# Kernel optimization log

Measured on AMD Instinct MI355X. Metric: run time of the kernel, lower is better.

The kernel has to match this reference:

```python
import jax, jax.numpy as jnp
import numpy as np

N_NODES = 200000   # total graph nodes (var + constraint)
N_VAR   = 112000   # nodes with x[:,0]==1, placed first for static slicing
N_EDGES = 3200000  # avg degree 16
HID     = 64
BATCH   = 64       # fc output width == batch_size in the torch module
TW      = 8        # target_width; TW*(TW-1)=56; N_VAR = seq_len*56 with seq_len=2000


def setup_inputs() -> dict:
    key = jax.random.key(0)
    ks = jax.random.split(key, 8)
    x = jax.random.normal(ks[0], (N_NODES, 2), jnp.float32)
    # var_mask = (x[:,0] == 1): make the first N_VAR nodes variable nodes.
    x = x.at[:, 0].set(jnp.where(jnp.arange(N_NODES) < N_VAR, 1.0, 0.0))
    edge_index = jax.random.randint(ks[1], (2, N_EDGES), 0, N_NODES, jnp.int32)
    W1 = jax.random.normal(ks[2], (2, HID), jnp.float32) / np.sqrt(2.0)
    b1 = jnp.zeros((HID,), jnp.float32)
    W2 = jax.random.normal(ks[3], (HID, HID), jnp.float32) / np.sqrt(HID)
    b2 = jnp.zeros((HID,), jnp.float32)
    Wfc = jax.random.normal(ks[4], (HID, BATCH), jnp.float32) / np.sqrt(HID)
    bfc = jnp.zeros((BATCH,), jnp.float32)
    return {"x": x, "edge_index": edge_index, "W1": W1, "b1": b1,
            "W2": W2, "b2": b2, "Wfc": Wfc, "bfc": bfc}


def gcn_conv(x, src, dst, W, b):
    """PyG GCNConv: transform, then sym-normalized aggregation with self-loops."""
    h = x @ W                                   # [N, F_out]
    ones = jnp.ones(src.shape[0], x.dtype)
    deg = jax.ops.segment_sum(ones, dst, num_segments=N_NODES) + 1.0  # +1: self-loop
    dinv = jax.lax.rsqrt(deg)                   # deg >= 1, always safe
    norm = dinv[src] * dinv[dst]                # [E]
    agg = jax.ops.segment_sum(h[src] * norm[:, None], dst, num_segments=N_NODES)
    agg = agg + h * (dinv * dinv)[:, None]      # self-loop message, norm = dinv_i^2
    return agg + b


def reference(x, edge_index, W1, b1, W2, b2, Wfc, bfc):
    src, dst = edge_index[0], edge_index[1]
    h = jax.nn.relu(gcn_conv(x, src, dst, W1, b1))
    h = gcn_conv(h, src, dst, W2, b2)
    # var_mask == first N_VAR rows by construction (static slice for jit)
    out = jax.nn.relu(h[:N_VAR] @ Wfc + bfc)    # [N_VAR, BATCH]
    width = TW * (TW - 1)                       # 56
    seq_len = N_VAR // width                    # 2000
    return jnp.round(out.reshape(seq_len, BATCH, width))
```

## Files before the change

### kernel.cpp

```cpp
#include <hip/hip_runtime.h>
#include <math.h>

#define N_NODES 200000
#define N_VAR   112000
#define N_EDGES 3200000
#define NB_SCAN 782
#define CAP     64

#define NFINE    512
#define PSZ_F    391
#define FCAP     7168
#define BIN_CHUNK 4096
#define NB_BIN   782

typedef int v4i __attribute__((ext_vector_type(4)));

__device__ __forceinline__ float bcast_lane(float x, int lane) {
    return __int_as_float(__builtin_amdgcn_readlane(__float_as_int(x), lane));
}

__global__ void __launch_bounds__(512) k_bin(const int* __restrict__ src,
                                             const int* __restrict__ dst,
                                             int* __restrict__ bins,
                                             int* __restrict__ bcnt,
                                             const float* __restrict__ W2,
                                             const float* __restrict__ b2,
                                             const float* __restrict__ Wfc,
                                             const float* __restrict__ bfc,
                                             float* __restrict__ Wc,
                                             float* __restrict__ bc) {
    __shared__ int hist[NFINE];
    __shared__ int seg[NFINE];
    __shared__ int gb[NFINE];
    __shared__ int cur[NFINE];
    __shared__ int wsum[8];
    __shared__ int stg[BIN_CHUNK];
    __shared__ unsigned short stgb[BIN_CHUNK];
    int tid = threadIdx.x;
    int lane = tid & 63, wid = tid >> 6;
    hist[tid] = 0;
    __syncthreads();

    int base = blockIdx.x * BIN_CHUNK;
    int pk[2][4];
    int bk[2][4];
    bool val[2];
    #pragma unroll
    for (int i = 0; i < 2; ++i) {
        int e4 = base + (i * 512 + tid) * 4;
        val[i] = (e4 < N_EDGES);
        if (val[i]) {
            v4i d = __builtin_nontemporal_load((const v4i*)(dst + e4));
            v4i s = __builtin_nontemporal_load((const v4i*)(src + e4));
            int dd[4] = {d.x, d.y, d.z, d.w};
            int ss[4] = {s.x, s.y, s.z, s.w};
            #pragma unroll
            for (int q = 0; q < 4; ++q) {
                int bb2 = dd[q] / PSZ_F;
                int dl = dd[q] - bb2 * PSZ_F;
                pk[i][q] = (dl << 18) | ss[q];
                bk[i][q] = bb2;
                atomicAdd(&hist[bb2], 1);
            }
        }
    }
    __syncthreads();

    int h = hist[tid];
    int inc = h;
    #pragma unroll
    for (int d = 1; d < 64; d <<= 1) {
        int t = __shfl_up(inc, d);
        if (lane >= d) inc += t;
    }
    if (lane == 63) wsum[wid] = inc;
    __syncthreads();
    int pre = 0, tot = 0;
    #pragma unroll
    for (int k = 0; k < 8; ++k) {
        int s = wsum[k];
        pre += (k < wid) ? s : 0;
        tot += s;
    }
    int ex = pre + inc - h;
    seg[tid] = ex;
    cur[tid] = ex;
    gb[tid]  = atomicAdd(&bcnt[tid], h);
    __syncthreads();

    #pragma unroll
    for (int i = 0; i < 2; ++i) {
        if (val[i]) {
            #pragma unroll
            for (int q = 0; q < 4; ++q) {
                int p = atomicAdd(&cur[bk[i][q]], 1);
                stg[p]  = pk[i][q];
                stgb[p] = (unsigned short)bk[i][q];
            }
        }
    }
    __syncthreads();

    for (int i = tid; i < tot; i += 512) {
        int bb2 = stgb[i];
        int pos = gb[bb2] + (i - seg[bb2]);
        if (pos < FCAP)
            bins[(size_t)bb2 * FCAP + pos] = stg[i];
    }

    int b = blockIdx.x;
    if (b < 8) {
        int e = b * 512 + tid;
        int j = e >> 6, l2 = e & 63;
        double acc = 0.0;
        for (int m = 0; m < 64; ++m)
            acc += (double)W2[j * 64 + m] * (double)Wfc[m * 64 + l2];
        Wc[e] = (float)acc;
    } else if (b == 8 && tid < 64) {
        double acc = (double)bfc[tid];
        for (int m = 0; m < 64; ++m)
            acc += (double)b2[m] * (double)Wfc[m * 64 + tid];
        bc[tid] = (float)acc;
    }
}

__global__ void __launch_bounds__(512) k_sort(const int* __restrict__ bins,
                                              const int* __restrict__ bcnt,
                                              const float2* __restrict__ x2,
                                              int* __restrict__ cnt,
                                              float4* __restrict__ xdc,
                                              int* __restrict__ buf) {
    __shared__ int hist[NFINE];
    __shared__ int off[NFINE];
    __shared__ int cur[NFINE];
    __shared__ int wsum[8];
    __shared__ int sorted[FCAP];
    __shared__ unsigned short rowid[FCAP];
    int tid = threadIdx.x;
    int lane = tid & 63, wid = tid >> 6;
    int b = blockIdx.x;
    int n = bcnt[b];
    if (n > FCAP) n = FCAP;
    const int* __restrict__ bp = bins + (size_t)b * FCAP;

    hist[tid] = 0;
    __syncthreads();
    for (int i = tid; i < n; i += 512)
        atomicAdd(&hist[bp[i] >> 18], 1);
    __syncthreads();

    int h = hist[tid];

    int vg = b * PSZ_F + tid;
    if (tid < PSZ_F && vg < N_NODES) {
        cnt[vg] = h;
        float dvv = rsqrtf((float)h + 1.0f);
        float2 xv = x2[vg];
        xdc[vg] = make_float4(xv.x * dvv, xv.y * dvv, dvv, 0.0f);
    }

    int inc = h;
    #pragma unroll
    for (int d = 1; d < 64; d <<= 1) {
        int t = __shfl_up(inc, d);
        if (lane >= d) inc += t;
    }
    if (lane == 63) wsum[wid] = inc;
    __syncthreads();
    int pre = 0;
    #pragma unroll
    for (int k = 0; k < 8; ++k) {
        int s = wsum[k];
        pre += (k < wid) ? s : 0;
    }
    int ex = pre + inc - h;
    off[tid] = ex;
    cur[tid] = ex;
    __syncthreads();

    for (int i = tid; i < n; i += 512) {
        int pkv = bp[i];
        int dl = pkv >> 18;
        int p = atomicAdd(&cur[dl], 1);
        sorted[p] = pkv & 0x3FFFF;
        rowid[p]  = (unsigned short)dl;
    }
    __syncthreads();

    for (int i = tid; i < n; i += 512) {
        int dl = rowid[i];
        int slot = i - off[dl];
        if (slot < CAP)
            buf[(size_t)(b * PSZ_F + dl) * CAP + slot] = sorted[i];
    }
}

__global__ void __launch_bounds__(256) k_l1a(const int* __restrict__ cnt,
                                             const int* __restrict__ buf,
                                             const float4* __restrict__ xdc,
                                             float4* __restrict__ zn) {
    int v = blockIdx.x * 256 + threadIdx.x;
    if (v >= N_NODES) return;
    int c = cnt[v];
    int n = (c < CAP) ? c : CAP;
    const int* __restrict__ rowp = buf + v * CAP;
    float4 self = xdc[v];
    float dv = self.z;
    float ax = self.x, ay = self.y;
    float bx = 0.0f,   by = 0.0f;
    int j = 0;
    for (; j + 16 <= n; j += 16) {
        v4i r0 = __builtin_nontemporal_load((const v4i*)(rowp + j));
        v4i r1 = __builtin_nontemporal_load((const v4i*)(rowp + j + 4));
        v4i r2 = __builtin_nontemporal_load((const v4i*)(rowp + j + 8));
        v4i r3 = __builtin_nontemporal_load((const v4i*)(rowp + j + 12));
        float4 p0 = xdc[r0.x], p1 = xdc[r0.y], p2 = xdc[r0.z], p3 = xdc[r0.w];
        float4 p4 = xdc[r1.x], p5 = xdc[r1.y], p6 = xdc[r1.z], p7 = xdc[r1.w];
        float4 p8 = xdc[r2.x], p9 = xdc[r2.y], pa = xdc[r2.z], pb = xdc[r2.w];
        float4 pc = xdc[r3.x], pd = xdc[r3.y], pe = xdc[r3.z], pf = xdc[r3.w];
        ax += p0.x; ay += p0.y;  bx += p1.x; by += p1.y;
        ax += p2.x; ay += p2.y;  bx += p3.x; by += p3.y;
        ax += p4.x; ay += p4.y;  bx += p5.x; by += p5.y;
        ax += p6.x; ay += p6.y;  bx += p7.x; by += p7.y;
        ax += p8.x; ay += p8.y;  bx += p9.x; by += p9.y;
        ax += pa.x; ay += pa.y;  bx += pb.x; by += pb.y;
        ax += pc.x; ay += pc.y;  bx += pd.x; by += pd.y;
        ax += pe.x; ay += pe.y;  bx += pf.x; by += pf.y;
    }
    for (; j + 8 <= n; j += 8) {
        v4i r0 = __builtin_nontemporal_load((const v4i*)(rowp + j));
        v4i r1 = __builtin_nontemporal_load((const v4i*)(rowp + j + 4));
        float4 p0 = xdc[r0.x], p1 = xdc[r0.y], p2 = xdc[r0.z], p3 = xdc[r0.w];
        float4 p4 = xdc[r1.x], p5 = xdc[r1.y], p6 = xdc[r1.z], p7 = xdc[r1.w];
        ax += p0.x; ay += p0.y;  bx += p1.x; by += p1.y;
        ax += p2.x; ay += p2.y;  bx += p3.x; by += p3.y;
        ax += p4.x; ay += p4.y;  bx += p5.x; by += p5.y;
        ax += p6.x; ay += p6.y;  bx += p7.x; by += p7.y;
    }
    for (; j < n; ++j) {
        int s = rowp[j];
        float4 p = xdc[s];
        ax += p.x; ay += p.y;
    }
    zn[v] = make_float4((ax + bx) * dv, (ay + by) * dv, dv, 0.0f);
}

__global__ void __launch_bounds__(256, 4) k_l2(const int* __restrict__ cnt,
                                               const int* __restrict__ buf,
                                               const float4* __restrict__ zn,
                                               const float* __restrict__ W1,
                                               const float* __restrict__ b1,
                                               const float* __restrict__ Wc,
                                               const float* __restrict__ bc,
                                               float* __restrict__ out) {
    int w = threadIdx.x >> 6, l = threadIdx.x & 63;
    float wc[64];
    #pragma unroll
    for (int jv = 0; jv < 64; ++jv)
        wc[jv] = Wc[jv * 64 + l];
    float w1a = W1[l], w1b = W1[64 + l], bb = b1[l];
    float bcl = bc[l];
    int v0 = blockIdx.x * 16 + w;
    int cc0 = __builtin_amdgcn_readfirstlane(cnt[v0]);
    int cc1 = __builtin_amdgcn_readfirstlane(cnt[v0 + 4]);
    int cc2 = __builtin_amdgcn_readfirstlane(cnt[v0 + 8]);
    int cc3 = __builtin_amdgcn_readfirstlane(cnt[v0 + 12]);

    int nn[4];
    float4 p[4], zs[4];
    #pragma unroll
    for (int it = 0; it < 4; ++it) {
        int v = v0 + it * 4;
        int c = (it == 0) ? cc0 : (it == 1) ? cc1 : (it == 2) ? cc2 : cc3;
        int n = (c < CAP) ? c : CAP;
        nn[it] = n;
        int ridx = __builtin_nontemporal_load(buf + v * CAP + l);
        int idx  = (l < n) ? ridx : v;
        p[it]  = zn[idx];
        zs[it] = zn[v];
    }

    #pragma unroll
    for (int it = 0; it < 4; ++it) {
        int v = v0 + it * 4;
        int c = (it == 0) ? cc0 : (it == 1) ? cc1 : (it == 2) ? cc2 : cc3;
        int n = nn[it];
        float dv = rsqrtf((float)c + 1.0f);
        float4 pp = p[it];
        float4 zss = zs[it];

        float acc0 = fmaxf(fmaf(zss.x, w1a, fmaf(zss.y, w1b, bb)), 0.0f) * zss.z;
        float acc1 = 0.0f;
        int j = 0;
        for (; j + 8 <= n; j += 8) {
            float x0 = bcast_lane(pp.x, j+0), y0 = bcast_lane(pp.y, j+0), z0 = bcast_lane(pp.z, j+0);
            float x1 = bcast_lane(pp.x, j+1), y1 = bcast_lane(pp.y, j+1), z1 = bcast_lane(pp.z, j+1);
            float x2 = bcast_lane(pp.x, j+2), y2 = bcast_lane(pp.y, j+2), z2 = bcast_lane(pp.z, j+2);
            float x3 = bcast_lane(pp.x, j+3), y3 = bcast_lane(pp.y, j+3), z3 = bcast_lane(pp.z, j+3);
            float x4 = bcast_lane(pp.x, j+4), y4 = bcast_lane(pp.y, j+4), z4 = bcast_lane(pp.z, j+4);
            float x5 = bcast_lane(pp.x, j+5), y5 = bcast_lane(pp.y, j+5), z5 = bcast_lane(pp.z, j+5);
            float x6 = bcast_lane(pp.x, j+6), y6 = bcast_lane(pp.y, j+6), z6 = bcast_lane(pp.z, j+6);
            float x7 = bcast_lane(pp.x, j+7), y7 = bcast_lane(pp.y, j+7), z7 = bcast_lane(pp.z, j+7);
            float h0 = fmaxf(fmaf(x0, w1a, fmaf(y0, w1b, bb)), 0.0f) * z0;
            float h1 = fmaxf(fmaf(x1, w1a, fmaf(y1, w1b, bb)), 0.0f) * z1;
            float h2 = fmaxf(fmaf(x2, w1a, fmaf(y2, w1b, bb)), 0.0f) * z2;
            float h3 = fmaxf(fmaf(x3, w1a, fmaf(y3, w1b, bb)), 0.0f) * z3;
            float h4 = fmaxf(fmaf(x4, w1a, fmaf(y4, w1b, bb)), 0.0f) * z4;
            float h5 = fmaxf(fmaf(x5, w1a, fmaf(y5, w1b, bb)), 0.0f) * z5;
            float h6 = fmaxf(fmaf(x6, w1a, fmaf(y6, w1b, bb)), 0.0f) * z6;
            float h7 = fmaxf(fmaf(x7, w1a, fmaf(y7, w1b, bb)), 0.0f) * z7;
            acc0 += (h0 + h1) + (h2 + h3);
            acc1 += (h4 + h5) + (h6 + h7);
        }
        for (; j + 4 <= n; j += 4) {
            float x0 = bcast_lane(pp.x, j+0), y0 = bcast_lane(pp.y, j+0), z0 = bcast_lane(pp.z, j+0);
            float x1 = bcast_lane(pp.x, j+1), y1 = bcast_lane(pp.y, j+1), z1 = bcast_lane(pp.z, j+1);
            float x2 = bcast_lane(pp.x, j+2), y2 = bcast_lane(pp.y, j+2), z2 = bcast_lane(pp.z, j+2);
            float x3 = bcast_lane(pp.x, j+3), y3 = bcast_lane(pp.y, j+3), z3 = bcast_lane(pp.z, j+3);
            float h0 = fmaxf(fmaf(x0, w1a, fmaf(y0, w1b, bb)), 0.0f) * z0;
            float h1 = fmaxf(fmaf(x1, w1a, fmaf(y1, w1b, bb)), 0.0f) * z1;
            float h2 = fmaxf(fmaf(x2, w1a, fmaf(y2, w1b, bb)), 0.0f) * z2;
            float h3 = fmaxf(fmaf(x3, w1a, fmaf(y3, w1b, bb)), 0.0f) * z3;
            acc0 += (h0 + h1) + (h2 + h3);
        }
        for (; j < n; ++j) {
            float xk = bcast_lane(pp.x, j), yk = bcast_lane(pp.y, j), zk = bcast_lane(pp.z, j);
            acc1 += fmaxf(fmaf(xk, w1a, fmaf(yk, w1b, bb)), 0.0f) * zk;
        }
        float Av = (acc0 + acc1) * dv;

        float t0 = 0.0f, t1 = 0.0f, t2 = 0.0f, t3 = 0.0f;
        #pragma unroll
        for (int jj = 0; jj < 64; jj += 4) {
            t0 = fmaf(bcast_lane(Av, jj + 0), wc[jj + 0], t0);
            t1 = fmaf(bcast_lane(Av, jj + 1), wc[jj + 1], t1);
            t2 = fmaf(bcast_lane(Av, jj + 2), wc[jj + 2], t2);
            t3 = fmaf(bcast_lane(Av, jj + 3), wc[jj + 3], t3);
        }
        float t = ((t0 + t1) + (t2 + t3)) + bcl;
        __builtin_nontemporal_store(rintf(fmaxf(t, 0.0f)), out + v * 64 + l);
    }
}


extern "C" void kernel_launch(void* const* d_in, const int* in_sizes, int n_in,
                              void* d_out, int out_size, void* d_ws, size_t ws_size,
                              hipStream_t stream) {
    const float* x    = (const float*)d_in[0];
    const int*   ei   = (const int*)  d_in[1];
    const float* W1   = (const float*)d_in[2];
    const float* b1   = (const float*)d_in[3];
    const float* W2   = (const float*)d_in[4];
    const float* b2   = (const float*)d_in[5];
    const float* Wfc  = (const float*)d_in[6];
    const float* bfc  = (const float*)d_in[7];
    float* out = (float*)d_out;

    const int* src = ei;
    const int* dst = ei + N_EDGES;

    char* ws = (char*)d_ws;
    int*    cnt    = (int*)   (ws + 0);
    float4* xdc    = (float4*)(ws + 800000);
    int*    bins   = (int*)   (ws + 4000000);
    int*    bcnt   = (int*)   (ws + 18680064);
    float4* zn     = (float4*)(ws + 15204096);
    int*    buf    = (int*)   (ws + 19204096);
    float*  Wc     = (float*) (ws + 70404096);
    float*  bc     = (float*) (ws + 70420480);

    hipMemsetAsync(bcnt, 0, NFINE * sizeof(int), stream);
    k_bin  <<<NB_BIN, 512, 0, stream>>>(src, dst, bins, bcnt, W2, b2, Wfc, bfc, Wc, bc);
    k_sort <<<NFINE, 512, 0, stream>>>(bins, bcnt, (const float2*)x, cnt, xdc, buf);
    k_l1a  <<<NB_SCAN, 256, 0, stream>>>(cnt, buf, xdc, zn);
    k_l2   <<<N_VAR / 16, 256, 0, stream>>>(cnt, buf, zn, W1, b1, Wc, bc, out);
}
```

Before: 225.4 us.

## Batch fc matvec across four nodes, pad neighbor loop, enlarge bin chunk

In k_l2, the 64-entry per-lane Wc register array is removed. Each Wc element is now loaded once per jj and used for four node vectors at the same time, which cuts register pressure and may allow higher occupancy. Neighbor slots beyond the count are zeroed, so the layer-1 aggregation loop runs in whole steps of 8 with no tail loops. In k_bin, each block now handles 8192 edges instead of 4096, halving the block count and the global atomics on bcnt, at the cost of more registers per thread and more staging shared memory.

```diff
diff --git a/kernel.cpp b/kernel.cpp
--- a/kernel.cpp
+++ b/kernel.cpp
@@ -10,8 +10,8 @@
 #define NFINE    512
 #define PSZ_F    391
 #define FCAP     7168
-#define BIN_CHUNK 4096
-#define NB_BIN   782
+#define BIN_CHUNK 8192
+#define NB_BIN   391
 
 typedef int v4i __attribute__((ext_vector_type(4)));
 
@@ -42,11 +42,11 @@
     __syncthreads();
 
     int base = blockIdx.x * BIN_CHUNK;
-    int pk[2][4];
-    int bk[2][4];
-    bool val[2];
-    #pragma unroll
-    for (int i = 0; i < 2; ++i) {
+    int pk[4][4];
+    int bk[4][4];
+    bool val[4];
+    #pragma unroll
+    for (int i = 0; i < 4; ++i) {
         int e4 = base + (i * 512 + tid) * 4;
         val[i] = (e4 < N_EDGES);
         if (val[i]) {
@@ -89,7 +89,7 @@
     __syncthreads();
 
     #pragma unroll
-    for (int i = 0; i < 2; ++i) {
+    for (int i = 0; i < 4; ++i) {
         if (val[i]) {
             #pragma unroll
             for (int q = 0; q < 4; ++q) {
@@ -254,10 +254,6 @@
                                                const float* __restrict__ bc,
                                                float* __restrict__ out) {
     int w = threadIdx.x >> 6, l = threadIdx.x & 63;
-    float wc[64];
-    #pragma unroll
-    for (int jv = 0; jv < 64; ++jv)
-        wc[jv] = Wc[jv * 64 + l];
     float w1a = W1[l], w1b = W1[64 + l], bb = b1[l];
     float bcl = bc[l];
     int v0 = blockIdx.x * 16 + w;
@@ -276,23 +272,24 @@
         nn[it] = n;
         int ridx = __builtin_nontemporal_load(buf + v * CAP + l);
         int idx  = (l < n) ? ridx : v;
-        p[it]  = zn[idx];
+        float4 t = zn[idx];
+        if (l >= n) { t.x = 0.0f; t.y = 0.0f; t.z = 0.0f; }
+        p[it]  = t;
         zs[it] = zn[v];
     }
 
+    float Av[4];
     #pragma unroll
     for (int it = 0; it < 4; ++it) {
-        int v = v0 + it * 4;
         int c = (it == 0) ? cc0 : (it == 1) ? cc1 : (it == 2) ? cc2 : cc3;
-        int n = nn[it];
         float dv = rsqrtf((float)c + 1.0f);
+        int n8 = (nn[it] + 7) & ~7;
         float4 pp = p[it];
         float4 zss = zs[it];
 
         float acc0 = fmaxf(fmaf(zss.x, w1a, fmaf(zss.y, w1b, bb)), 0.0f) * zss.z;
         float acc1 = 0.0f;
-        int j = 0;
-        for (; j + 8 <= n; j += 8) {
+        for (int j = 0; j < n8; j += 8) {
             float x0 = bcast_lane(pp.x, j+0), y0 = bcast_lane(pp.y, j+0), z0 = bcast_lane(pp.z, j+0);
             float x1 = bcast_lane(pp.x, j+1), y1 = bcast_lane(pp.y, j+1), z1 = bcast_lane(pp.z, j+1);
             float x2 = bcast_lane(pp.x, j+2), y2 = bcast_lane(pp.y, j+2), z2 = bcast_lane(pp.z, j+2);
@@ -312,32 +309,29 @@
             acc0 += (h0 + h1) + (h2 + h3);
             acc1 += (h4 + h5) + (h6 + h7);
         }
-        for (; j + 4 <= n; j += 4) {
-            float x0 = bcast_lane(pp.x, j+0), y0 = bcast_lane(pp.y, j+0), z0 = bcast_lane(pp.z, j+0);
-            float x1 = bcast_lane(pp.x, j+1), y1 = bcast_lane(pp.y, j+1), z1 = bcast_lane(pp.z, j+1);
-            float x2 = bcast_lane(pp.x, j+2), y2 = bcast_lane(pp.y, j+2), z2 = bcast_lane(pp.z, j+2);
-            float x3 = bcast_lane(pp.x, j+3), y3 = bcast_lane(pp.y, j+3), z3 = bcast_lane(pp.z, j+3);
-            float h0 = fmaxf(fmaf(x0, w1a, fmaf(y0, w1b, bb)), 0.0f) * z0;
-            float h1 = fmaxf(fmaf(x1, w1a, fmaf(y1, w1b, bb)), 0.0f) * z1;
-            float h2 = fmaxf(fmaf(x2, w1a, fmaf(y2, w1b, bb)), 0.0f) * z2;
-            float h3 = fmaxf(fmaf(x3, w1a, fmaf(y3, w1b, bb)), 0.0f) * z3;
-            acc0 += (h0 + h1) + (h2 + h3);
+        Av[it] = (acc0 + acc1) * dv;
+    }
+
+    float t0[4] = {0.f,0.f,0.f,0.f}, t1[4] = {0.f,0.f,0.f,0.f};
+    float t2[4] = {0.f,0.f,0.f,0.f}, t3[4] = {0.f,0.f,0.f,0.f};
+    #pragma unroll
+    for (int jj = 0; jj < 64; jj += 4) {
+        float wc0 = Wc[(jj + 0) * 64 + l];
+        float wc1 = Wc[(jj + 1) * 64 + l];
+        float wc2 = Wc[(jj + 2) * 64 + l];
+        float wc3 = Wc[(jj + 3) * 64 + l];
+        #pragma unroll
+        for (int it = 0; it < 4; ++it) {
+            t0[it] = fmaf(bcast_lane(Av[it], jj + 0), wc0, t0[it]);
+            t1[it] = fmaf(bcast_lane(Av[it], jj + 1), wc1, t1[it]);
+            t2[it] = fmaf(bcast_lane(Av[it], jj + 2), wc2, t2[it]);
+            t3[it] = fmaf(bcast_lane(Av[it], jj + 3), wc3, t3[it]);
         }
-        for (; j < n; ++j) {
-            float xk = bcast_lane(pp.x, j), yk = bcast_lane(pp.y, j), zk = bcast_lane(pp.z, j);
-            acc1 += fmaxf(fmaf(xk, w1a, fmaf(yk, w1b, bb)), 0.0f) * zk;
-        }
-        float Av = (acc0 + acc1) * dv;
-
-        float t0 = 0.0f, t1 = 0.0f, t2 = 0.0f, t3 = 0.0f;
-        #pragma unroll
-        for (int jj = 0; jj < 64; jj += 4) {
-            t0 = fmaf(bcast_lane(Av, jj + 0), wc[jj + 0], t0);
-            t1 = fmaf(bcast_lane(Av, jj + 1), wc[jj + 1], t1);
-            t2 = fmaf(bcast_lane(Av, jj + 2), wc[jj + 2], t2);
-            t3 = fmaf(bcast_lane(Av, jj + 3), wc[jj + 3], t3);
-        }
-        float t = ((t0 + t1) + (t2 + t3)) + bcl;
+    }
+    #pragma unroll
+    for (int it = 0; it < 4; ++it) {
+        int v = v0 + it * 4;
+        float t = ((t0[it] + t1[it]) + (t2[it] + t3[it])) + bcl;
         __builtin_nontemporal_store(rintf(fmaxf(t, 0.0f)), out + v * 64 + l);
     }
 }
```

New measurement: 227.3 us. Within noise of the previous version (+0.8%).
